# Kernel tuning notes

Hardware: AMD Instinct MI355X
Metric: run time of the kernel (lower is better)

## Reference

```python
import jax, jax.numpy as jnp
import numpy as np

D = 1024
H = 16
DK = D // H


def apply_rope(x):
    # x: [B, H, T, dk]; interleaved-pair RoPE as in the torch source
    T, dim = x.shape[-2], x.shape[-1]
    inv_freq = 1.0 / (10000.0 ** (jnp.arange(0, dim, 2, dtype=x.dtype) / dim))  # [dk/2]
    pos = jnp.arange(T, dtype=x.dtype)
    sinusoid = pos[:, None] * inv_freq[None, :]  # [T, dk/2]
    sin, cos = jnp.sin(sinusoid), jnp.cos(sinusoid)
    x1, x2 = x[..., ::2], x[..., 1::2]
    rot = jnp.stack([x1 * cos - x2 * sin, x1 * sin + x2 * cos], axis=-1)
    return rot.reshape(x.shape)


def setup_inputs() -> dict:
    key = jax.random.key(0)
    k1, k2, k3, k4, k5 = jax.random.split(key, 5)
    B, T = 2, 2048
    s = 1.0 / np.sqrt(D)
    return {
        "x": jax.random.normal(k1, (B, T, D), dtype=jnp.float32),
        "W_qkv": jax.random.normal(k2, (D, 3 * D), dtype=jnp.float32) * s,
        "b_qkv": jnp.zeros((3 * D,), dtype=jnp.float32),
        "W_out": jax.random.normal(k3, (D, D), dtype=jnp.float32) * s,
        "b_out": jnp.zeros((D,), dtype=jnp.float32),
    }


def reference(x, W_qkv, b_qkv, W_out, b_out):
    B, T, C = x.shape
    qkv = x @ W_qkv + b_qkv  # [B, T, 3D]
    qkv = qkv.reshape(B, T, 3, H, DK).transpose(2, 0, 3, 1, 4)  # [3, B, H, T, dk]
    q, k, v = qkv[0], qkv[1], qkv[2]
    q, k = apply_rope(q), apply_rope(k)
    scores = jnp.einsum("bhtd,bhsd->bhts", q, k) / jnp.sqrt(jnp.asarray(DK, x.dtype))
    causal = jnp.tril(jnp.ones((T, T), dtype=bool))
    scores = jnp.where(causal, scores, jnp.asarray(-1e9, x.dtype))
    probs = jax.nn.softmax(scores, axis=-1)
    attn = jnp.einsum("bhts,bhsd->bhtd", probs, v)  # [B, H, T, dk]
    out = attn.transpose(0, 2, 1, 3).reshape(B, T, C)  # b h t d -> b t (h d)
    return out @ W_out + b_out
```

## Files before the change

kernel.cpp:

```cpp
#include <hip/hip_runtime.h>
#include <math.h>

#define DMODEL 1024
#define NHEAD  16
#define HDK    64
#define BATCH  2
#define SEQ    2048
#define MROWS  (BATCH*SEQ)
#define NQKV   (3*DMODEL)
#define LOG2_10000 13.287712379549449f
#define INV2PI 0.15915494309189535f
#define SCALE_LOG2E 0.1803368801111137f
#define M_FIX 8.0f

typedef __attribute__((ext_vector_type(8))) short bf16x8;
typedef __attribute__((ext_vector_type(4))) short s16x4;
typedef __attribute__((ext_vector_type(4))) float f32x4;
typedef __attribute__((ext_vector_type(2))) unsigned int u32x2;

__device__ __forceinline__ short f2bf(float f) {
    union { float f; unsigned u; } v; v.f = f;
    unsigned r = v.u + 0x7fffu + ((v.u >> 16) & 1u);
    return (short)(r >> 16);
}

__device__ __forceinline__ float fast_exp2(float x) {
#if __has_builtin(__builtin_amdgcn_exp2f)
    return __builtin_amdgcn_exp2f(x);
#else
    return exp2f(x);
#endif
}

__device__ __forceinline__ void gld_lds16(const short* g, short* l) {
    __builtin_amdgcn_global_load_lds(
        (const __attribute__((address_space(1))) void*)g,
        (__attribute__((address_space(3))) void*)l, 16, 0, 0);
}

__global__ __launch_bounds__(256) void prep_kernel(
    const float* __restrict__ x, const float* __restrict__ wqkv,
    const float* __restrict__ wout,
    short* __restrict__ xb, short* __restrict__ wqkv_t, short* __restrict__ wout_t)
{
    __shared__ short tile[32][33];
    const int tid = threadIdx.x;
    if (blockIdx.x < 2048) {
        const int i = (blockIdx.x * 256 + tid) * 8;
        float4 a = *(const float4*)(x + i);
        float4 b = *(const float4*)(x + i + 4);
        bf16x8 o;
        o[0] = f2bf(a.x); o[1] = f2bf(a.y); o[2] = f2bf(a.z); o[3] = f2bf(a.w);
        o[4] = f2bf(b.x); o[5] = f2bf(b.y); o[6] = f2bf(b.z); o[7] = f2bf(b.w);
        *(bf16x8*)(xb + i) = o;
        return;
    }
    const int bx = blockIdx.x - 2048;
    int nx = bx & 127;
    const int ky = bx >> 7;
    const float* in; short* out; int N;
    if (nx < 96) { in = wqkv; out = wqkv_t; N = NQKV; }
    else         { in = wout; out = wout_t; N = DMODEL; nx -= 96; }
    const int tx = tid & 31, ty = tid >> 5;
    const int n0 = nx * 32, k0 = ky * 32;
    #pragma unroll
    for (int i = 0; i < 32; i += 8)
        tile[ty + i][tx] = f2bf(in[(size_t)(k0 + ty + i) * N + n0 + tx]);
    __syncthreads();
    #pragma unroll
    for (int i = 0; i < 32; i += 8)
        out[(size_t)(n0 + ty + i) * DMODEL + k0 + tx] = tile[tx][ty + i];
}

__global__ __launch_bounds__(256) void qkv_gemm_kernel(
    const short* __restrict__ xb, const short* __restrict__ Wt,
    const float* __restrict__ bias,
    short* __restrict__ qd, short* __restrict__ kd, short* __restrict__ vtb)
{
    __shared__ __align__(16) short As[2][128 * 32];
    __shared__ __align__(16) short Bs[2][128 * 32];
    const int tid = threadIdx.x;
    const int lane = tid & 63, wave = tid >> 6;
    const int wm = wave & 1, wn = wave >> 1;
    const int l15 = lane & 15, quad = lane >> 4;
    const int n0 = blockIdx.x * 128, m0 = blockIdx.y * 128;
    const int srow = lane >> 2, sc = lane & 3;
    const int scp = sc ^ ((srow >> 1) & 3);
    const int rdx = (l15 >> 1) & 3;

    const short* gA1 = xb + (size_t)(m0 + wave * 32 + srow) * DMODEL + scp * 8;
    const short* gA2 = gA1 + (size_t)16 * DMODEL;
    const short* gB1 = Wt + (size_t)(n0 + wave * 32 + srow) * DMODEL + scp * 8;
    const short* gB2 = gB1 + (size_t)16 * DMODEL;
    const int lofsA1 = (wave * 32) * 32;
    const int lofsA2 = (wave * 32 + 16) * 32;

    f32x4 zero = {0.f, 0.f, 0.f, 0.f};
    f32x4 acc[4][4];
    #pragma unroll
    for (int i = 0; i < 4; ++i)
        #pragma unroll
        for (int j = 0; j < 4; ++j) acc[i][j] = zero;

    gld_lds16(gA1, As[0] + lofsA1);
    gld_lds16(gA2, As[0] + lofsA2);
    gld_lds16(gB1, Bs[0] + lofsA1);
    gld_lds16(gB2, Bs[0] + lofsA2);
    __syncthreads();

    for (int k = 0; k < DMODEL / 32; ++k) {
        const int cur = k & 1;
        if (k + 1 < DMODEL / 32) {
            const int kn = (k + 1) * 32;
            gld_lds16(gA1 + kn, As[cur ^ 1] + lofsA1);
            gld_lds16(gA2 + kn, As[cur ^ 1] + lofsA2);
            gld_lds16(gB1 + kn, Bs[cur ^ 1] + lofsA1);
            gld_lds16(gB2 + kn, Bs[cur ^ 1] + lofsA2);
        }
        bf16x8 af[4], bfr[4];
        #pragma unroll
        for (int i = 0; i < 4; ++i)
            af[i] = *(const bf16x8*)&As[cur][(wm * 64 + i * 16 + l15) * 32 + (quad ^ rdx) * 8];
        #pragma unroll
        for (int j = 0; j < 4; ++j)
            bfr[j] = *(const bf16x8*)&Bs[cur][(wn * 64 + j * 16 + l15) * 32 + (quad ^ rdx) * 8];
        #pragma unroll
        for (int i = 0; i < 4; ++i)
            #pragma unroll
            for (int j = 0; j < 4; ++j)
                acc[i][j] = __builtin_amdgcn_mfma_f32_16x16x32_bf16(af[i], bfr[j], acc[i][j], 0, 0, 0);
        __syncthreads();
    }

    const int which = n0 >> 10;
    float biasv[4], invf[4];
    int hh[4], dd[4];
    #pragma unroll
    for (int j = 0; j < 4; ++j) {
        const int n = n0 + wn * 64 + j * 16 + l15;
        biasv[j] = bias[n];
        hh[j] = (n & 1023) >> 6;
        dd[j] = n & 63;
        invf[j] = INV2PI * exp2f(-((float)(dd[j] & ~1) / 64.f) * LOG2_10000);
    }
    #pragma unroll
    for (int i = 0; i < 4; ++i) {
        const int mb = m0 + wm * 64 + i * 16 + quad * 4;
        const int b = mb >> 11, tb = mb & (SEQ - 1);
        if (which < 2) {
            #pragma unroll
            for (int j = 0; j < 4; ++j) {
                #pragma unroll
                for (int r = 0; r < 4; ++r) {
                    const int t = tb + r;
                    float val = acc[i][j][r] + biasv[j];
                    const float rev = (float)t * invf[j];
                    const float fr = rev - floorf(rev);
                    const float s = __builtin_amdgcn_sinf(fr);
                    const float c = __builtin_amdgcn_cosf(fr);
                    const float partner = __shfl_xor(val, 1);
                    val = (lane & 1) ? (partner * s + val * c) : (val * c - partner * s);
                    short* dst = (which == 0) ? qd : kd;
                    dst[((size_t)(b * NHEAD + hh[j]) * SEQ + t) * HDK + dd[j]] = f2bf(val);
                }
            }
        } else {
            #pragma unroll
            for (int j = 0; j < 4; ++j) {
                s16x4 sv;
                #pragma unroll
                for (int r = 0; r < 4; ++r)
                    sv[r] = f2bf(acc[i][j][r] + biasv[j]);
                *(s16x4*)&vtb[((size_t)(b * NHEAD + hh[j]) * HDK + dd[j]) * SEQ + tb] = sv;
            }
        }
    }
}

__global__ __launch_bounds__(512) void attn_mfma_kernel(
    const short* __restrict__ qd, const short* __restrict__ kd,
    const short* __restrict__ vt, short* __restrict__ od)
{
    __shared__ __align__(16) short Ks[2][2][64 * 32];
    __shared__ __align__(16) short Vs[2][2][64 * 32];
    __shared__ __align__(16) short Ps[8][16 * 64];
    const int tid = threadIdx.x, lane = tid & 63, w = tid >> 6;
    const int l15 = lane & 15, quad = lane >> 4;
    const int par = w >> 2;
    const int ws = w & 3;
    const int id = (int)blockIdx.x;
    const int c = id & 7, g = id >> 3;
    const int qt = 31 - (g >> 2);
    const int jj = g & 3;
    const int hb = c + 8 * jj;
    const int h = hb & 15, b = hb >> 4;
    const size_t base = ((size_t)(b * NHEAD + h)) * SEQ * HDK;
    const int stid = tid & 255;
    const int hi = tid >> 8;
    const int srow = stid >> 2, sc = stid & 3;
    const int lofs = srow * 32 + (sc ^ ((srow >> 1) & 3)) * 8;
    const int rdx = (l15 >> 1) & 3;
    const int pmask = (l15 & 3) << 2;
    f32x4 zero = {0.f, 0.f, 0.f, 0.f};

    const short* kp = kd + base + (size_t)(hi * 64 + srow) * HDK + sc * 8;
    const short* vp = vt + base + (size_t)srow * SEQ + hi * 64 + sc * 8;

    const int q0 = qt * 64;
    const int trow = q0 + ws * 16 + l15;
    bf16x8 qf[2];
    {
        const short* qrow = qd + base + (size_t)trow * HDK;
        qf[0] = *(const bf16x8*)(qrow + quad * 8);
        qf[1] = *(const bf16x8*)(qrow + 32 + quad * 8);
    }
    float l_acc = 0.f;
    f32x4 o[4];
    #pragma unroll
    for (int j = 0; j < 4; ++j) o[j] = zero;

    const int nkt = qt + 1;
    const int npair = (nkt + 1) >> 1;
    short* myPs = &Ps[w][0];

    bf16x8 rk[2], rv[2];
    rk[0] = *(const bf16x8*)kp; rk[1] = *(const bf16x8*)(kp + 32);
    rv[0] = *(const bf16x8*)vp; rv[1] = *(const bf16x8*)(vp + 32);

    for (int p = 0; p < npair; ++p) {
        __syncthreads();
        *(bf16x8*)&Ks[hi][0][lofs] = rk[0];
        *(bf16x8*)&Ks[hi][1][lofs] = rk[1];
        *(bf16x8*)&Vs[hi][0][lofs] = rv[0];
        *(bf16x8*)&Vs[hi][1][lofs] = rv[1];
        __syncthreads();
        if (p + 1 < npair) {
            const int sn = (2 * p + 2) * 64;
            const short* kn = kp + (size_t)sn * HDK;
            const short* vn = vp + sn;
            rk[0] = *(const bf16x8*)kn; rk[1] = *(const bf16x8*)(kn + 32);
            rv[0] = *(const bf16x8*)vn; rv[1] = *(const bf16x8*)(vn + 32);
        }

        const int kt = 2 * p + par;
        if (kt < nkt) {
            f32x4 sacc[4];
            #pragma unroll
            for (int j = 0; j < 4; ++j) {
                const int ro = (j * 16 + l15) * 32 + (quad ^ rdx) * 8;
                bf16x8 kf0 = *(const bf16x8*)&Ks[par][0][ro];
                bf16x8 kf1 = *(const bf16x8*)&Ks[par][1][ro];
                sacc[j] = __builtin_amdgcn_mfma_f32_16x16x32_bf16(kf0, qf[0], zero, 0, 0, 0);
                sacc[j] = __builtin_amdgcn_mfma_f32_16x16x32_bf16(kf1, qf[1], sacc[j], 0, 0, 0);
            }
            if (kt == nkt - 1) {
                const int s0 = kt * 64;
                #pragma unroll
                for (int j = 0; j < 4; ++j) {
                    float pv[4];
                    #pragma unroll
                    for (int r = 0; r < 4; ++r) {
                        const int scol = s0 + j * 16 + quad * 4 + r;
                        const float sv = sacc[j][r] * SCALE_LOG2E - M_FIX;
                        pv[r] = (scol > trow) ? 0.f : fast_exp2(sv);
                        l_acc += pv[r];
                    }
                    unsigned pk0, pk1;
                    asm("v_cvt_pk_bf16_f32 %0, %1, %2" : "=v"(pk0) : "v"(pv[0]), "v"(pv[1]));
                    asm("v_cvt_pk_bf16_f32 %0, %1, %2" : "=v"(pk1) : "v"(pv[2]), "v"(pv[3]));
                    const int cc = (j * 4 + quad) ^ pmask;
                    u32x2 pkv = {pk0, pk1};
                    *(u32x2*)&myPs[l15 * 64 + cc * 4] = pkv;
                }
            } else {
                #pragma unroll
                for (int j = 0; j < 4; ++j) {
                    float pv[4];
                    #pragma unroll
                    for (int r = 0; r < 4; ++r) {
                        pv[r] = fast_exp2(sacc[j][r] * SCALE_LOG2E - M_FIX);
                        l_acc += pv[r];
                    }
                    unsigned pk0, pk1;
                    asm("v_cvt_pk_bf16_f32 %0, %1, %2" : "=v"(pk0) : "v"(pv[0]), "v"(pv[1]));
                    asm("v_cvt_pk_bf16_f32 %0, %1, %2" : "=v"(pk1) : "v"(pv[2]), "v"(pv[3]));
                    const int cc = (j * 4 + quad) ^ pmask;
                    u32x2 pkv = {pk0, pk1};
                    *(u32x2*)&myPs[l15 * 64 + cc * 4] = pkv;
                }
            }
            bf16x8 pf0 = *(const bf16x8*)&myPs[l15 * 64 + ((quad * 2) ^ pmask) * 4];
            bf16x8 pf1 = *(const bf16x8*)&myPs[l15 * 64 + ((8 + quad * 2) ^ pmask) * 4];
            #pragma unroll
            for (int j = 0; j < 4; ++j) {
                const int ro = (j * 16 + l15) * 32 + (quad ^ rdx) * 8;
                bf16x8 vf0 = *(const bf16x8*)&Vs[par][0][ro];
                bf16x8 vf1 = *(const bf16x8*)&Vs[par][1][ro];
                o[j] = __builtin_amdgcn_mfma_f32_16x16x32_bf16(pf0, vf0, o[j], 0, 0, 0);
                o[j] = __builtin_amdgcn_mfma_f32_16x16x32_bf16(pf1, vf1, o[j], 0, 0, 0);
            }
        }
    }

    float sr = l_acc;
    sr += __shfl_xor(sr, 16);
    sr += __shfl_xor(sr, 32);

    __syncthreads();
    float* ob   = (float*)&Ks[0][0][0];
    float* lbuf = (float*)&Vs[0][0][0];
    lbuf[w * 16 + l15] = sr;
    if (par == 1) {
        const int bi = (ws * 64 + lane) * 16;
        #pragma unroll
        for (int j = 0; j < 4; ++j)
            #pragma unroll
            for (int r = 0; r < 4; ++r) ob[bi + j * 4 + r] = o[j][r];
    }
    __syncthreads();
    if (par == 0) {
        const int bi = (ws * 64 + lane) * 16;
        #pragma unroll
        for (int j = 0; j < 4; ++j)
            #pragma unroll
            for (int r = 0; r < 4; ++r) o[j][r] += ob[bi + j * 4 + r];

        #pragma unroll
        for (int r = 0; r < 4; ++r) {
            const int qq = quad * 4 + r;
            const float lt = lbuf[ws * 16 + qq] + lbuf[(ws + 4) * 16 + qq];
            const float inv = 1.f / lt;
            const int t = q0 + ws * 16 + qq;
            #pragma unroll
            for (int j = 0; j < 4; ++j)
                od[((size_t)(b * SEQ + t) * NHEAD + h) * HDK + j * 16 + l15] =
                    f2bf(o[j][r] * inv);
        }
    }
}

__global__ __launch_bounds__(256) void out_gemm_kernel(
    const short* __restrict__ Ab, const short* __restrict__ Wt,
    const float* __restrict__ bias, float* __restrict__ out)
{
    __shared__ __align__(16) short As[2][128 * 32];
    __shared__ __align__(16) short Bs[2][64 * 32];
    const int tid = threadIdx.x;
    const int lane = tid & 63, wave = tid >> 6;
    const int wm = wave & 1, wn = wave >> 1;
    const int l15 = lane & 15, quad = lane >> 4;
    const int n0 = blockIdx.x * 64, m0 = blockIdx.y * 128;
    const int srow = lane >> 2, sc = lane & 3;
    const int scp = sc ^ ((srow >> 1) & 3);
    const int rdx = (l15 >> 1) & 3;

    const short* gA1 = Ab + (size_t)(m0 + wave * 32 + srow) * DMODEL + scp * 8;
    const short* gA2 = gA1 + (size_t)16 * DMODEL;
    const short* gB1 = Wt + (size_t)(n0 + wave * 16 + srow) * DMODEL + scp * 8;
    const int lofsA1 = (wave * 32) * 32;
    const int lofsA2 = (wave * 32 + 16) * 32;
    const int lofsB  = (wave * 16) * 32;

    f32x4 zero = {0.f, 0.f, 0.f, 0.f};
    f32x4 acc[4][2];
    #pragma unroll
    for (int i = 0; i < 4; ++i)
        #pragma unroll
        for (int j = 0; j < 2; ++j) acc[i][j] = zero;

    gld_lds16(gA1, As[0] + lofsA1);
    gld_lds16(gA2, As[0] + lofsA2);
    gld_lds16(gB1, Bs[0] + lofsB);
    __syncthreads();

    for (int k = 0; k < DMODEL / 32; ++k) {
        const int cur = k & 1;
        if (k + 1 < DMODEL / 32) {
            const int kn = (k + 1) * 32;
            gld_lds16(gA1 + kn, As[cur ^ 1] + lofsA1);
            gld_lds16(gA2 + kn, As[cur ^ 1] + lofsA2);
            gld_lds16(gB1 + kn, Bs[cur ^ 1] + lofsB);
        }
        bf16x8 af[4], bfr[2];
        #pragma unroll
        for (int i = 0; i < 4; ++i)
            af[i] = *(const bf16x8*)&As[cur][(wm * 64 + i * 16 + l15) * 32 + (quad ^ rdx) * 8];
        #pragma unroll
        for (int j = 0; j < 2; ++j)
            bfr[j] = *(const bf16x8*)&Bs[cur][(wn * 32 + j * 16 + l15) * 32 + (quad ^ rdx) * 8];
        #pragma unroll
        for (int i = 0; i < 4; ++i)
            #pragma unroll
            for (int j = 0; j < 2; ++j)
                acc[i][j] = __builtin_amdgcn_mfma_f32_16x16x32_bf16(af[i], bfr[j], acc[i][j], 0, 0, 0);
        __syncthreads();
    }

    #pragma unroll
    for (int j = 0; j < 2; ++j) {
        const int n = n0 + wn * 32 + j * 16 + l15;
        const float bv = bias[n];
        #pragma unroll
        for (int i = 0; i < 4; ++i)
            #pragma unroll
            for (int r = 0; r < 4; ++r) {
                const int m = m0 + wm * 64 + i * 16 + quad * 4 + r;
                out[(size_t)m * DMODEL + n] = acc[i][j][r] + bv;
            }
    }
}

extern "C" void kernel_launch(void* const* d_in, const int* in_sizes, int n_in,
                              void* d_out, int out_size, void* d_ws, size_t ws_size,
                              hipStream_t stream) {
    const float* x    = (const float*)d_in[0];
    const float* Wqkv = (const float*)d_in[1];
    const float* bqkv = (const float*)d_in[2];
    const float* Wout = (const float*)d_in[3];
    const float* bout = (const float*)d_in[4];
    float* out = (float*)d_out;

    short* ws = (short*)d_ws;
    short* xb     = ws;
    short* wqkv_t = xb + (size_t)4 * 1024 * 1024;
    short* wout_t = wqkv_t + (size_t)3 * 1024 * 1024;
    short* qd     = wout_t + (size_t)1024 * 1024;
    short* kd     = qd + (size_t)4 * 1024 * 1024;
    short* vtb    = kd + (size_t)4 * 1024 * 1024;
    short* attn   = vtb + (size_t)4 * 1024 * 1024;

    prep_kernel<<<2048 + 4096, 256, 0, stream>>>(x, Wqkv, Wout, xb, wqkv_t, wout_t);

    qkv_gemm_kernel<<<dim3(NQKV / 128, MROWS / 128), 256, 0, stream>>>(
        xb, wqkv_t, bqkv, qd, kd, vtb);

    attn_mfma_kernel<<<1024, 512, 0, stream>>>(qd, kd, vtb, attn);

    out_gemm_kernel<<<dim3(DMODEL / 64, MROWS / 128), 256, 0, stream>>>(
        attn, wout_t, bout, out);
}
```

Baseline: 176.0 us.

## Triple-buffer LDS in QKV and output GEMMs with fine-grained vmcnt waits

Both projection GEMMs move from a double-buffered LDS pipeline with __syncthreads to a three-stage ring, prefetching two K-tiles ahead. Each step uses an explicit s_waitcnt vmcnt(N) plus s_barrier so that only the oldest tile's loads have to land before compute, keeping more global-to-LDS traffic in flight. This costs 50% more shared memory per block, which can lower occupancy. It also depends on the compiler not reordering LDS reads across the raw inline-asm barriers.

```diff
diff --git a/kernel.cpp b/kernel.cpp
--- a/kernel.cpp
+++ b/kernel.cpp
@@ -77,8 +77,8 @@
     const float* __restrict__ bias,
     short* __restrict__ qd, short* __restrict__ kd, short* __restrict__ vtb)
 {
-    __shared__ __align__(16) short As[2][128 * 32];
-    __shared__ __align__(16) short Bs[2][128 * 32];
+    __shared__ __align__(16) short As[3][128 * 32];
+    __shared__ __align__(16) short Bs[3][128 * 32];
     const int tid = threadIdx.x;
     const int lane = tid & 63, wave = tid >> 6;
     const int wm = wave & 1, wn = wave >> 1;
@@ -102,35 +102,51 @@
         #pragma unroll
         for (int j = 0; j < 4; ++j) acc[i][j] = zero;
 
-    gld_lds16(gA1, As[0] + lofsA1);
-    gld_lds16(gA2, As[0] + lofsA2);
-    gld_lds16(gB1, Bs[0] + lofsA1);
-    gld_lds16(gB2, Bs[0] + lofsA2);
-    __syncthreads();
-
-    for (int k = 0; k < DMODEL / 32; ++k) {
-        const int cur = k & 1;
-        if (k + 1 < DMODEL / 32) {
-            const int kn = (k + 1) * 32;
-            gld_lds16(gA1 + kn, As[cur ^ 1] + lofsA1);
-            gld_lds16(gA2 + kn, As[cur ^ 1] + lofsA2);
-            gld_lds16(gB1 + kn, Bs[cur ^ 1] + lofsA1);
-            gld_lds16(gB2 + kn, Bs[cur ^ 1] + lofsA2);
-        }
-        bf16x8 af[4], bfr[4];
-        #pragma unroll
-        for (int i = 0; i < 4; ++i)
-            af[i] = *(const bf16x8*)&As[cur][(wm * 64 + i * 16 + l15) * 32 + (quad ^ rdx) * 8];
-        #pragma unroll
-        for (int j = 0; j < 4; ++j)
-            bfr[j] = *(const bf16x8*)&Bs[cur][(wn * 64 + j * 16 + l15) * 32 + (quad ^ rdx) * 8];
-        #pragma unroll
-        for (int i = 0; i < 4; ++i)
-            #pragma unroll
-            for (int j = 0; j < 4; ++j)
-                acc[i][j] = __builtin_amdgcn_mfma_f32_16x16x32_bf16(af[i], bfr[j], acc[i][j], 0, 0, 0);
-        __syncthreads();
-    }
+#define QKV_COMPUTE(CUR)                                                          \
+    {                                                                             \
+        bf16x8 af[4], bfr[4];                                                     \
+        _Pragma("unroll")                                                         \
+        for (int i = 0; i < 4; ++i)                                               \
+            af[i] = *(const bf16x8*)&As[CUR][(wm * 64 + i * 16 + l15) * 32 + (quad ^ rdx) * 8]; \
+        _Pragma("unroll")                                                         \
+        for (int j = 0; j < 4; ++j)                                               \
+            bfr[j] = *(const bf16x8*)&Bs[CUR][(wn * 64 + j * 16 + l15) * 32 + (quad ^ rdx) * 8]; \
+        _Pragma("unroll")                                                         \
+        for (int i = 0; i < 4; ++i)                                               \
+            _Pragma("unroll")                                                     \
+            for (int j = 0; j < 4; ++j)                                           \
+                acc[i][j] = __builtin_amdgcn_mfma_f32_16x16x32_bf16(af[i], bfr[j], acc[i][j], 0, 0, 0); \
+    }
+
+    gld_lds16(gA1, &As[0][lofsA1]);
+    gld_lds16(gA2, &As[0][lofsA2]);
+    gld_lds16(gB1, &Bs[0][lofsA1]);
+    gld_lds16(gB2, &Bs[0][lofsA2]);
+    gld_lds16(gA1 + 32, &As[1][lofsA1]);
+    gld_lds16(gA2 + 32, &As[1][lofsA2]);
+    gld_lds16(gB1 + 32, &Bs[1][lofsA1]);
+    gld_lds16(gB2 + 32, &Bs[1][lofsA2]);
+
+    int cur = 0, nx = 2;
+    #pragma unroll 3
+    for (int k = 0; k < 30; ++k) {
+        const int kn = (k + 2) * 32;
+        gld_lds16(gA1 + kn, &As[nx][lofsA1]);
+        gld_lds16(gA2 + kn, &As[nx][lofsA2]);
+        gld_lds16(gB1 + kn, &Bs[nx][lofsA1]);
+        gld_lds16(gB2 + kn, &Bs[nx][lofsA2]);
+        asm volatile("s_waitcnt vmcnt(8)\n\ts_barrier" ::: "memory");
+        QKV_COMPUTE(cur);
+        asm volatile("s_barrier" ::: "memory");
+        cur = (cur == 2) ? 0 : cur + 1;
+        nx  = (nx == 2) ? 0 : nx + 1;
+    }
+    asm volatile("s_waitcnt vmcnt(4)\n\ts_barrier" ::: "memory");
+    QKV_COMPUTE(cur);
+    cur = (cur == 2) ? 0 : cur + 1;
+    asm volatile("s_waitcnt vmcnt(0)\n\ts_barrier" ::: "memory");
+    QKV_COMPUTE(cur);
+#undef QKV_COMPUTE
 
     const int which = n0 >> 10;
     float biasv[4], invf[4];
@@ -343,8 +359,8 @@
     const short* __restrict__ Ab, const short* __restrict__ Wt,
     const float* __restrict__ bias, float* __restrict__ out)
 {
-    __shared__ __align__(16) short As[2][128 * 32];
-    __shared__ __align__(16) short Bs[2][64 * 32];
+    __shared__ __align__(16) short As[3][128 * 32];
+    __shared__ __align__(16) short Bs[3][64 * 32];
     const int tid = threadIdx.x;
     const int lane = tid & 63, wave = tid >> 6;
     const int wm = wave & 1, wn = wave >> 1;
@@ -368,33 +384,48 @@
         #pragma unroll
         for (int j = 0; j < 2; ++j) acc[i][j] = zero;
 
-    gld_lds16(gA1, As[0] + lofsA1);
-    gld_lds16(gA2, As[0] + lofsA2);
-    gld_lds16(gB1, Bs[0] + lofsB);
-    __syncthreads();
-
-    for (int k = 0; k < DMODEL / 32; ++k) {
-        const int cur = k & 1;
-        if (k + 1 < DMODEL / 32) {
-            const int kn = (k + 1) * 32;
-            gld_lds16(gA1 + kn, As[cur ^ 1] + lofsA1);
-            gld_lds16(gA2 + kn, As[cur ^ 1] + lofsA2);
-            gld_lds16(gB1 + kn, Bs[cur ^ 1] + lofsB);
-        }
-        bf16x8 af[4], bfr[2];
-        #pragma unroll
-        for (int i = 0; i < 4; ++i)
-            af[i] = *(const bf16x8*)&As[cur][(wm * 64 + i * 16 + l15) * 32 + (quad ^ rdx) * 8];
-        #pragma unroll
-        for (int j = 0; j < 2; ++j)
-            bfr[j] = *(const bf16x8*)&Bs[cur][(wn * 32 + j * 16 + l15) * 32 + (quad ^ rdx) * 8];
-        #pragma unroll
-        for (int i = 0; i < 4; ++i)
-            #pragma unroll
-            for (int j = 0; j < 2; ++j)
-                acc[i][j] = __builtin_amdgcn_mfma_f32_16x16x32_bf16(af[i], bfr[j], acc[i][j], 0, 0, 0);
-        __syncthreads();
-    }
+#define OUT_COMPUTE(CUR)                                                          \
+    {                                                                             \
+        bf16x8 af[4], bfr[2];                                                     \
+        _Pragma("unroll")                                                         \
+        for (int i = 0; i < 4; ++i)                                               \
+            af[i] = *(const bf16x8*)&As[CUR][(wm * 64 + i * 16 + l15) * 32 + (quad ^ rdx) * 8]; \
+        _Pragma("unroll")                                                         \
+        for (int j = 0; j < 2; ++j)                                               \
+            bfr[j] = *(const bf16x8*)&Bs[CUR][(wn * 32 + j * 16 + l15) * 32 + (quad ^ rdx) * 8]; \
+        _Pragma("unroll")                                                         \
+        for (int i = 0; i < 4; ++i)                                               \
+            _Pragma("unroll")                                                     \
+            for (int j = 0; j < 2; ++j)                                           \
+                acc[i][j] = __builtin_amdgcn_mfma_f32_16x16x32_bf16(af[i], bfr[j], acc[i][j], 0, 0, 0); \
+    }
+
+    gld_lds16(gA1, &As[0][lofsA1]);
+    gld_lds16(gA2, &As[0][lofsA2]);
+    gld_lds16(gB1, &Bs[0][lofsB]);
+    gld_lds16(gA1 + 32, &As[1][lofsA1]);
+    gld_lds16(gA2 + 32, &As[1][lofsA2]);
+    gld_lds16(gB1 + 32, &Bs[1][lofsB]);
+
+    int cur = 0, nx = 2;
+    #pragma unroll 3
+    for (int k = 0; k < 30; ++k) {
+        const int kn = (k + 2) * 32;
+        gld_lds16(gA1 + kn, &As[nx][lofsA1]);
+        gld_lds16(gA2 + kn, &As[nx][lofsA2]);
+        gld_lds16(gB1 + kn, &Bs[nx][lofsB]);
+        asm volatile("s_waitcnt vmcnt(6)\n\ts_barrier" ::: "memory");
+        OUT_COMPUTE(cur);
+        asm volatile("s_barrier" ::: "memory");
+        cur = (cur == 2) ? 0 : cur + 1;
+        nx  = (nx == 2) ? 0 : nx + 1;
+    }
+    asm volatile("s_waitcnt vmcnt(3)\n\ts_barrier" ::: "memory");
+    OUT_COMPUTE(cur);
+    cur = (cur == 2) ? 0 : cur + 1;
+    asm volatile("s_waitcnt vmcnt(0)\n\ts_barrier" ::: "memory");
+    OUT_COMPUTE(cur);
+#undef OUT_COMPUTE
 
     #pragma unroll
     for (int j = 0; j < 2; ++j) {
```

Result: slower. 186.4 us (+5.9%).
